# Kernel optimization log

Measured on AMD Instinct MI355X. Metric: run time of the kernel, lower is better.

The kernel has to match this reference:

```python
import jax, jax.numpy as jnp
import numpy as np

H, W = 32, 56
CK, CV = 64, 512
N = 16 * H * W  # long + work memory fully populated: 16 frames of H*W entries
TOP_K = 30


def setup_inputs() -> dict:
    key = jax.random.key(0)
    k1, k2, k3, k4, k5 = jax.random.split(key, 5)
    return {
        "q_key": jax.random.normal(k1, (1, CK, H, W), dtype=jnp.float32),
        "q_selection": jax.random.uniform(k2, (1, CK, H, W), dtype=jnp.float32),
        "mem_key": jax.random.normal(k3, (1, CK, N), dtype=jnp.float32),
        "mem_shrinkage": jax.random.uniform(k4, (1, N, 1), dtype=jnp.float32),
        "mem_value": jax.random.normal(k5, (2, CV, N), dtype=jnp.float32),
    }


def reference(q_key, q_selection, mem_key, mem_shrinkage, mem_value):
    b, ck, h, w = q_key.shape
    hw = h * w
    qk = q_key.reshape(1, ck, hw)          # [1, CK, HW]
    qs = q_selection.reshape(1, ck, hw)    # [1, CK, HW]

    mk = jnp.swapaxes(mem_key, 1, 2)       # [1, N, CK]
    # negative weighted squared L2 distance via matmul algebra
    a_sq = jnp.matmul(mk * mk, qs)                    # [1, N, HW]
    two_ab = 2.0 * jnp.matmul(mk, qk * qs)            # [1, N, HW]
    b_sq = jnp.sum(qs * qk * qk, axis=1, keepdims=True)  # [1, 1, HW]
    sim = (-a_sq + two_ab - b_sq) * mem_shrinkage / jnp.sqrt(jnp.float32(ck))  # [1, N, HW]

    # topk over the memory axis (dim=1), softmax over selected entries, scatter back
    simT = jnp.swapaxes(sim, 1, 2)                    # [1, HW, N]
    vals, idx = jax.lax.top_k(simT, TOP_K)            # [1, HW, K]
    x_exp = jnp.exp(vals)
    x_exp = x_exp / jnp.sum(x_exp, axis=-1, keepdims=True)
    i0 = jnp.arange(1)[:, None, None]
    i1 = jnp.arange(hw)[None, :, None]
    affT = jnp.zeros_like(simT).at[i0, i1, idx].set(x_exp)  # [1, HW, N]
    affinity = jnp.swapaxes(affT, 1, 2)               # [1, N, HW]

    out = jnp.matmul(mem_value, affinity)             # [2, CV, HW] (batch-broadcast)
    return out.reshape(2, CV, h, w)
```

## Files before the change

### kernel.cpp

```cpp
#include <hip/hip_runtime.h>
#include <math.h>

#define HW      1792
#define NMEM    28672
#define NCHUNK  3584
#define TOPK    30
#define CTARGET 48
#define SCAP    64
#define FINCAP  64
#define SIMB    448
#define WPS     7
#define NSELB   448

typedef __attribute__((ext_vector_type(8))) short bf16x8;
typedef __attribute__((ext_vector_type(8))) unsigned short u16x8;
typedef __attribute__((ext_vector_type(4))) float f32x4;
typedef __attribute__((ext_vector_type(4))) _Float16 h4;
typedef unsigned long long ull;

static __device__ __forceinline__ unsigned short f2bf(float v) {
  unsigned b = __float_as_uint(v);
  return (unsigned short)((b + 0x7FFFu + ((b >> 16) & 1u)) >> 16);
}
static __device__ __forceinline__ float bf2f(unsigned short h) {
  return __uint_as_float(((unsigned)h) << 16);
}
static __device__ __forceinline__ unsigned fkey(float v) {
  return __float_as_uint(-v) & 0x7FFFFFFFu;
}
static __device__ __forceinline__ void gl_lds16(const void* g, void* l) {
  __builtin_amdgcn_global_load_lds(
      (const __attribute__((address_space(1))) unsigned*)g,
      (__attribute__((address_space(3))) unsigned*)l, 16, 0, 0);
}
#define WSYNC() do { asm volatile("s_waitcnt lgkmcnt(0)" ::: "memory"); \
                     __builtin_amdgcn_wave_barrier(); } while (0)

__global__ __launch_bounds__(256)
void k_prep_b(const float* __restrict__ mk, const float* __restrict__ shr_in,
              unsigned short* __restrict__ Bh,
              float* __restrict__ mkT, float* __restrict__ shr_s)
{
  const int n = blockIdx.x * 256 + threadIdx.x;
  shr_s[n] = shr_in[n] * 0.125f;
  for (int cb = 0; cb < 64; cb += 8) {
    u16x8 h1, h2;
    float vv[8];
    #pragma unroll
    for (int j = 0; j < 8; ++j) {
      float v = mk[(size_t)(cb + j) * NMEM + n];
      vv[j] = v;
      h1[j] = f2bf(v);
      h2[j] = f2bf(v * v);
    }
    const int s = cb >> 3;
    *reinterpret_cast<u16x8*>(&Bh[((size_t)s * NMEM + n) * 8])       = h1;
    *reinterpret_cast<u16x8*>(&Bh[((size_t)(s + 8) * NMEM + n) * 8]) = h2;
    *reinterpret_cast<float4*>(&mkT[(size_t)n * 64 + cb])     = make_float4(vv[0], vv[1], vv[2], vv[3]);
    *reinterpret_cast<float4*>(&mkT[(size_t)n * 64 + cb + 4]) = make_float4(vv[4], vv[5], vv[6], vv[7]);
  }
}

__global__ __launch_bounds__(256)
void k_prep_u(const float* __restrict__ q_key, const float* __restrict__ q_sel,
              unsigned short* __restrict__ Uh, unsigned short* __restrict__ Ul,
              float* __restrict__ bsq)
{
  const int p = blockIdx.x * 256 + threadIdx.x;
  float bs = 0.f;
  for (int cb = 0; cb < 64; cb += 8) {
    u16x8 h1, l1, h2, l2;
    #pragma unroll
    for (int j = 0; j < 8; ++j) {
      int c = cb + j;
      float k = q_key[(size_t)c * HW + p];
      float s = q_sel[(size_t)c * HW + p];
      float u = 2.f * k * s;
      float w = -s;
      bs = fmaf(s * k, k, bs);
      unsigned short h = f2bf(u); h1[j] = h; l1[j] = f2bf(u - bf2f(h));
      unsigned short g = f2bf(w); h2[j] = g; l2[j] = f2bf(w - bf2f(g));
    }
    const int s = cb >> 3;
    *reinterpret_cast<u16x8*>(&Uh[((size_t)s * HW + p) * 8])       = h1;
    *reinterpret_cast<u16x8*>(&Ul[((size_t)s * HW + p) * 8])       = l1;
    *reinterpret_cast<u16x8*>(&Uh[((size_t)(s + 8) * HW + p) * 8]) = h2;
    *reinterpret_cast<u16x8*>(&Ul[((size_t)(s + 8) * HW + p) * 8]) = l2;
  }
  bsq[p] = bs;
}

__global__ __launch_bounds__(256, 2)
void k_sim(const unsigned short* __restrict__ Uh, const unsigned short* __restrict__ Ul,
           const unsigned short* __restrict__ Bh,
           const float* __restrict__ bsq, const float* __restrict__ shr_s,
           float* __restrict__ pmax)
{
  __shared__ char smem[65536] __attribute__((aligned(16)));
  const int tid = threadIdx.x;
  const int wid = tid >> 6, lane = tid & 63;
  const int lr = lane & 15, lg = lane >> 4;
  const int pb = blockIdx.x % 14, st = blockIdx.x / 14;
  const int pw = pb * 128 + wid * 32;
  const int w0 = st * WPS;

  bf16x8 a0h[4], a0l[4], a1h[4], a1l[4];
  #pragma unroll
  for (int t = 0; t < 4; ++t) {
    const size_t e0 = ((size_t)(t * 4 + lg) * HW + pw + lr) * 8;
    const size_t e1 = e0 + 16 * 8;
    a0h[t] = *reinterpret_cast<const bf16x8*>(&Uh[e0]);
    a0l[t] = *reinterpret_cast<const bf16x8*>(&Ul[e0]);
    a1h[t] = *reinterpret_cast<const bf16x8*>(&Uh[e1]);
    a1l[t] = *reinterpret_cast<const bf16x8*>(&Ul[e1]);
  }
  float bq[2][4];
  #pragma unroll
  for (int pt = 0; pt < 2; ++pt)
    #pragma unroll
    for (int r = 0; r < 4; ++r) bq[pt][r] = bsq[pw + pt * 16 + 4 * lg + r];

  auto stage = [&](int buf, int i) {
    const int n0 = (w0 + i) * 128;
    #pragma unroll
    for (int j = 0; j < 8; ++j) {
      const int idx = j * 256 + tid;
      const int s = idx >> 7, rr = idx & 127;
      gl_lds16((const char*)Bh + ((size_t)s * NMEM + n0 + rr) * 16,
               smem + buf * 32768 + idx * 16);
    }
  };

  stage(0, 0);
  int buf = 0;
  for (int i = 0; i < WPS; ++i) {
    __syncthreads();
    if (i + 1 < WPS) stage(buf ^ 1, i + 1);

    f32x4 acc[2][8];
    #pragma unroll
    for (int a = 0; a < 2; ++a)
      #pragma unroll
      for (int b = 0; b < 8; ++b) acc[a][b] = (f32x4){0.f, 0.f, 0.f, 0.f};

    const short* lb = (const short*)(smem + buf * 32768);
    #pragma unroll
    for (int t = 0; t < 4; ++t) {
      #pragma unroll
      for (int nt = 0; nt < 8; ++nt) {
        bf16x8 bh = *reinterpret_cast<const bf16x8*>(
            &lb[((t * 4 + lg) * 128 + nt * 16 + lr) * 8]);
        acc[0][nt] = __builtin_amdgcn_mfma_f32_16x16x32_bf16(a0h[t], bh, acc[0][nt], 0, 0, 0);
        acc[0][nt] = __builtin_amdgcn_mfma_f32_16x16x32_bf16(a0l[t], bh, acc[0][nt], 0, 0, 0);
        acc[1][nt] = __builtin_amdgcn_mfma_f32_16x16x32_bf16(a1h[t], bh, acc[1][nt], 0, 0, 0);
        acc[1][nt] = __builtin_amdgcn_mfma_f32_16x16x32_bf16(a1l[t], bh, acc[1][nt], 0, 0, 0);
      }
    }

    const int wgl = w0 + i;
    const int n0 = wgl * 128;
    float shv[8];
    #pragma unroll
    for (int nt = 0; nt < 8; ++nt) shv[nt] = shr_s[n0 + nt * 16 + lr];
    #pragma unroll
    for (int pt = 0; pt < 2; ++pt) {
      #pragma unroll
      for (int r = 0; r < 4; ++r) {
        float mx = -INFINITY;
        #pragma unroll
        for (int nt = 0; nt < 8; ++nt)
          mx = fmaxf(mx, (acc[pt][nt][r] - bq[pt][r]) * shv[nt]);
        pmax[(size_t)(pw + pt * 16 + 4 * lg + r) * NCHUNK + wgl * 16 + lr] = mx;
      }
    }
    buf ^= 1;
  }
}

struct SelS {
  int   hist[4][512];
  ull   pk[4][512];
  ull   fin[4][FINCAP];
  short sl[4][SCAP];
  float sqk[4][64], sqs[4][64];
};
union SMemU { SelS sel; float tt[64][65]; };

static __device__ __forceinline__ int ph(int b) { return ((b & 7) << 6) | (b >> 3); }

static __device__ __forceinline__ void wave_cross8(const int* h, int lane, int target,
                                                   int& B, int& nA)
{
  int hv[8]; int ls = 0;
  #pragma unroll
  for (int k = 0; k < 8; ++k) { hv[k] = h[(k << 6) + lane]; ls += hv[k]; }
  int sc = ls;
  #pragma unroll
  for (int off = 1; off < 64; off <<= 1) {
    int t = __shfl_up(sc, off);
    if (lane >= off) sc += t;
  }
  int run = sc - ls;
  int myB = -1, mynA = 0;
  #pragma unroll
  for (int k = 0; k < 8; ++k) {
    if (run < target && run + hv[k] >= target) { myB = lane * 8 + k; mynA = run; }
    run += hv[k];
  }
  ull ball = __ballot(myB >= 0);
  int src = __ffsll((long long)ball) - 1;
  B = __shfl(myB, src); nA = __shfl(mynA, src);
}

__global__ __launch_bounds__(256, 4)
void k_selT(const float* __restrict__ pmax, const float* __restrict__ mkT,
            const float* __restrict__ q_key, const float* __restrict__ q_sel,
            const float* __restrict__ shr_s,
            float* __restrict__ wgt, int* __restrict__ widx,
            const float* __restrict__ mv, _Float16* __restrict__ mvT)
{
  __shared__ SMemU sm;
  const int tid = threadIdx.x;

  int sg = -1, tb = -1;
  if (gridDim.x > NSELB) {
    const int g = blockIdx.x / 17, r = blockIdx.x % 17;
    if (r == 0) sg = g; else tb = g * 16 + (r - 1);
  } else {
    sg = blockIdx.x;
  }

  if (tb >= 0) {
    const int n0 = (tb % 448) * 64, ch0 = (tb / 448) * 64;
    for (int i = tid; i < 64 * 16; i += 256) {
      int r = i >> 4, c4 = (i & 15) << 2;
      float4 v = *reinterpret_cast<const float4*>(&mv[(size_t)(ch0 + r) * NMEM + n0 + c4]);
      sm.tt[r][c4] = v.x; sm.tt[r][c4 + 1] = v.y;
      sm.tt[r][c4 + 2] = v.z; sm.tt[r][c4 + 3] = v.w;
    }
    __syncthreads();
    for (int i = tid; i < 64 * 16; i += 256) {
      int r = i >> 4, c4 = (i & 15) << 2;
      h4 hv = {(_Float16)sm.tt[c4][r], (_Float16)sm.tt[c4 + 1][r],
               (_Float16)sm.tt[c4 + 2][r], (_Float16)sm.tt[c4 + 3][r]};
      *reinterpret_cast<h4*>(&mvT[(size_t)(n0 + r) * 1024 + ch0 + c4]) = hv;
    }
    return;
  }

  const int w = tid >> 6, lane = tid & 63;
  const int pix = sg * 4 + w;
  int*   h  = sm.sel.hist[w];
  ull*   p  = sm.sel.pk[w];
  ull*   fin = sm.sel.fin[w];
  short* sl = sm.sel.sl[w];

  sm.sel.sqk[w][lane] = q_key[(size_t)lane * HW + pix];
  sm.sel.sqs[w][lane] = q_sel[(size_t)lane * HW + pix];

  float m[56];
  const float* pm = pmax + (size_t)pix * NCHUNK;
  #pragma unroll
  for (int j = 0; j < 56; ++j) m[j] = pm[lane + 64 * j];

  #pragma unroll
  for (int k = 0; k < 8; ++k) h[lane + 64 * k] = 0;
  WSYNC();
  #pragma unroll
  for (int j = 0; j < 56; ++j) atomicAdd(&h[ph(fkey(m[j]) >> 22)], 1);
  WSYNC();
  int B1, nA1;
  wave_cross8(h, lane, CTARGET, B1, nA1);

  #pragma unroll
  for (int k = 0; k < 8; ++k) h[lane + 64 * k] = 0;
  WSYNC();
  #pragma unroll
  for (int j = 0; j < 56; ++j) {
    unsigned u = fkey(m[j]);
    if ((int)(u >> 22) == B1) atomicAdd(&h[ph((u >> 13) & 511)], 1);
  }
  WSYNC();
  int Bs1, nAs1;
  wave_cross8(h, lane, CTARGET - nA1, Bs1, nAs1);

  int nsurv = 0;
  #pragma unroll
  for (int j = 0; j < 56; ++j) {
    unsigned u = fkey(m[j]);
    int b1 = (int)(u >> 22);
    bool keep = (b1 < B1) || (b1 == B1 && (int)((u >> 13) & 511) <= Bs1);
    ull ball = __ballot(keep);
    if (keep) {
      int pos = nsurv + __popcll(ball & ((1ull << lane) - 1ull));
      if (pos < SCAP) sl[pos] = (short)(lane + 64 * j);
    }
    nsurv += __popcll(ball);
  }
  nsurv = (nsurv < SCAP) ? nsurv : SCAP;
  const int NC = nsurv * 8;
  WSYNC();

  const float4* k4p = reinterpret_cast<const float4*>(sm.sel.sqk[w]);
  const float4* s4p = reinterpret_cast<const float4*>(sm.sel.sqs[w]);
  for (int c = lane; c < NC; c += 64) {
    const int cc = sl[c >> 3];
    const int n = ((cc >> 4) << 7) + (cc & 15) + ((c & 7) << 4);
    const float4* mr = reinterpret_cast<const float4*>(mkT + (size_t)n * 64);
    float s0 = 0.f, s1 = 0.f, s2 = 0.f, s3 = 0.f;
    #pragma unroll
    for (int j = 0; j < 4; ++j) {
      float4 q0 = mr[4 * j], q1 = mr[4 * j + 1], q2 = mr[4 * j + 2], q3 = mr[4 * j + 3];
      float4 a0 = k4p[4 * j], a1 = k4p[4 * j + 1], a2 = k4p[4 * j + 2], a3 = k4p[4 * j + 3];
      float4 b0 = s4p[4 * j], b1 = s4p[4 * j + 1], b2 = s4p[4 * j + 2], b3 = s4p[4 * j + 3];
      float d;
      d = q0.x - a0.x; s0 = fmaf(b0.x * d, d, s0);
      d = q0.y - a0.y; s1 = fmaf(b0.y * d, d, s1);
      d = q0.z - a0.z; s2 = fmaf(b0.z * d, d, s2);
      d = q0.w - a0.w; s3 = fmaf(b0.w * d, d, s3);
      d = q1.x - a1.x; s0 = fmaf(b1.x * d, d, s0);
      d = q1.y - a1.y; s1 = fmaf(b1.y * d, d, s1);
      d = q1.z - a1.z; s2 = fmaf(b1.z * d, d, s2);
      d = q1.w - a1.w; s3 = fmaf(b1.w * d, d, s3);
      d = q2.x - a2.x; s0 = fmaf(b2.x * d, d, s0);
      d = q2.y - a2.y; s1 = fmaf(b2.y * d, d, s1);
      d = q2.z - a2.z; s2 = fmaf(b2.z * d, d, s2);
      d = q2.w - a2.w; s3 = fmaf(b2.w * d, d, s3);
      d = q3.x - a3.x; s0 = fmaf(b3.x * d, d, s0);
      d = q3.y - a3.y; s1 = fmaf(b3.y * d, d, s1);
      d = q3.z - a3.z; s2 = fmaf(b3.z * d, d, s2);
      d = q3.w - a3.w; s3 = fmaf(b3.w * d, d, s3);
    }
    float v = -((s0 + s1) + (s2 + s3)) * shr_s[n];
    p[c] = ((ull)(0x7FFFFFFFu - fkey(v)) << 32) |
           (ull)(0xFFFFFFFFu - (unsigned)n);
  }
  WSYNC();

  #pragma unroll
  for (int k = 0; k < 8; ++k) h[lane + 64 * k] = 0;
  WSYNC();
  for (int c = lane; c < NC; c += 64) {
    unsigned qk = 0x7FFFFFFFu - (unsigned)(p[c] >> 32);
    atomicAdd(&h[ph(qk >> 22)], 1);
  }
  WSYNC();
  int B2, nA2;
  wave_cross8(h, lane, TOPK, B2, nA2);

  #pragma unroll
  for (int k = 0; k < 8; ++k) h[lane + 64 * k] = 0;
  WSYNC();
  for (int c = lane; c < NC; c += 64) {
    unsigned qk = 0x7FFFFFFFu - (unsigned)(p[c] >> 32);
    if ((int)(qk >> 22) == B2) atomicAdd(&h[ph((qk >> 13) & 511)], 1);
  }
  WSYNC();
  int Bs2, nAs2;
  wave_cross8(h, lane, TOPK - nA2, Bs2, nAs2);

  int nfin = 0;
  for (int c0 = 0; c0 < NC; c0 += 64) {
    int c = c0 + lane;
    bool isf = false; ull key = 0ull;
    if (c < NC) {
      key = p[c];
      unsigned qk = 0x7FFFFFFFu - (unsigned)(key >> 32);
      int b1 = (int)(qk >> 22);
      isf = (b1 < B2) || (b1 == B2 && (int)((qk >> 13) & 511) <= Bs2);
    }
    ull ball = __ballot(isf);
    if (isf) {
      int pos = nfin + __popcll(ball & ((1ull << lane) - 1ull));
      if (pos < FINCAP) fin[pos] = key;
    }
    nfin += __popcll(ball);
  }
  WSYNC();
  const int nf = (nfin < FINCAP) ? nfin : FINCAP;

  ull myk = (lane < nf) ? fin[lane] : 0ull;
  int r = 0;
  #pragma unroll
  for (int sft = 1; sft < 64; ++sft) {
    ull ok = __shfl_xor(myk, sft);
    r += (ok > myk) ? 1 : 0;
  }
  float v = -__uint_as_float(0x7FFFFFFFu - (unsigned)(myk >> 32));
  bool sel = (lane < nf) && (r < TOPK);
  float e = sel ? expf(v) : 0.f;
  float es = e;
  #pragma unroll
  for (int off = 32; off > 0; off >>= 1) es += __shfl_xor(es, off);
  if (sel) {
    wgt [(size_t)pix * 32 + r] = e / es;
    widx[(size_t)pix * 32 + r] = (int)(0xFFFFFFFFu - (unsigned)(myk & 0xFFFFFFFFu));
  }
}

__global__ __launch_bounds__(256)
void k_transpose_h(const float* __restrict__ mv, _Float16* __restrict__ mvT)
{
  __shared__ float t[64][65];
  const int n0 = blockIdx.x * 64, ch0 = blockIdx.y * 64;
  const int tid = threadIdx.x;
  for (int i = tid; i < 64 * 16; i += 256) {
    int r = i >> 4, c4 = (i & 15) << 2;
    float4 v = *reinterpret_cast<const float4*>(&mv[(size_t)(ch0 + r) * NMEM + n0 + c4]);
    t[r][c4] = v.x; t[r][c4 + 1] = v.y; t[r][c4 + 2] = v.z; t[r][c4 + 3] = v.w;
  }
  __syncthreads();
  for (int i = tid; i < 64 * 16; i += 256) {
    int r = i >> 4, c4 = (i & 15) << 2;
    h4 hv = {(_Float16)t[c4][r], (_Float16)t[c4 + 1][r],
             (_Float16)t[c4 + 2][r], (_Float16)t[c4 + 3][r]};
    *reinterpret_cast<h4*>(&mvT[(size_t)(n0 + r) * 1024 + ch0 + c4]) = hv;
  }
}

__global__ __launch_bounds__(256)
void k_gather_h(const _Float16* __restrict__ mvT, const float* __restrict__ wgt,
                const int* __restrict__ widx, float* __restrict__ out)
{
  __shared__ float sw[8][TOPK];
  __shared__ int   si[8][TOPK];
  __shared__ float sbuf[256][9];
  const int p0 = blockIdx.x * 8, chg = blockIdx.y * 256;
  const int tid = threadIdx.x;

  for (int i = tid; i < 8 * TOPK; i += 256) {
    int q = i / TOPK, k = i - q * TOPK;
    sw[q][k] = wgt [(size_t)(p0 + q) * 32 + k];
    si[q][k] = widx[(size_t)(p0 + q) * 32 + k];
  }
  __syncthreads();

  const int ch = chg + tid;
  #pragma unroll 2
  for (int q = 0; q < 8; ++q) {
    float a = 0.f;
    #pragma unroll
    for (int k = 0; k < TOPK; ++k)
      a = fmaf(sw[q][k], (float)mvT[(size_t)si[q][k] * 1024 + ch], a);
    sbuf[tid][q] = a;
  }
  __syncthreads();

  for (int i = tid; i < 256 * 8; i += 256) {
    int cl = i >> 3, q = i & 7;
    out[(size_t)(chg + cl) * HW + p0 + q] = sbuf[cl][q];
  }
}

__global__ __launch_bounds__(256)
void k_gather_f(const float* __restrict__ src, const float* __restrict__ wgt,
                const int* __restrict__ widx, float* __restrict__ out,
                long n_stride, long ch_stride)
{
  __shared__ float sw[8][TOPK];
  __shared__ int   si[8][TOPK];
  __shared__ float sbuf[256][9];
  const int p0 = blockIdx.x * 8, chg = blockIdx.y * 256;
  const int tid = threadIdx.x;

  for (int i = tid; i < 8 * TOPK; i += 256) {
    int q = i / TOPK, k = i - q * TOPK;
    sw[q][k] = wgt [(size_t)(p0 + q) * 32 + k];
    si[q][k] = widx[(size_t)(p0 + q) * 32 + k];
  }
  __syncthreads();

  const int ch = chg + tid;
  #pragma unroll 2
  for (int q = 0; q < 8; ++q) {
    float a = 0.f;
    #pragma unroll
    for (int k = 0; k < TOPK; ++k)
      a = fmaf(sw[q][k], src[(size_t)si[q][k] * n_stride + (size_t)ch * ch_stride], a);
    sbuf[tid][q] = a;
  }
  __syncthreads();

  for (int i = tid; i < 256 * 8; i += 256) {
    int cl = i >> 3, q = i & 7;
    out[(size_t)(chg + cl) * HW + p0 + q] = sbuf[cl][q];
  }
}

extern "C" void kernel_launch(void* const* d_in, const int* in_sizes, int n_in,
                              void* d_out, int out_size, void* d_ws, size_t ws_size,
                              hipStream_t stream)
{
  (void)in_sizes; (void)n_in; (void)out_size;
  const float* q_key     = (const float*)d_in[0];
  const float* q_sel     = (const float*)d_in[1];
  const float* mem_key   = (const float*)d_in[2];
  const float* mem_shr   = (const float*)d_in[3];
  const float* mem_value = (const float*)d_in[4];
  float* out = (float*)d_out;

  char* ws = (char*)d_ws;
  size_t off = 0;
  auto alloc = [&](size_t b) { size_t c = off; off = (off + b + 255) & ~(size_t)255; return c; };
  size_t o_w   = alloc((size_t)HW * 32 * 4);
  size_t o_wi  = alloc((size_t)HW * 32 * 4);
  size_t o_pr  = off;
  size_t o_bh  = alloc((size_t)NMEM * 128 * 2);
  size_t o_uh  = alloc((size_t)HW * 128 * 2);
  size_t o_ul  = alloc((size_t)HW * 128 * 2);
  size_t o_bsq = alloc((size_t)HW * 4);
  size_t o_shr = alloc((size_t)NMEM * 4);
  size_t o_mkT = alloc((size_t)NMEM * 64 * 4);
  size_t o_pm  = alloc((size_t)HW * NCHUNK * 4);
  size_t o_end = off;

  float*          wg   = (float*)(ws + o_w);
  int*            wi   = (int*)  (ws + o_wi);
  unsigned short* Bh   = (unsigned short*)(ws + o_bh);
  unsigned short* Uh   = (unsigned short*)(ws + o_uh);
  unsigned short* Ul   = (unsigned short*)(ws + o_ul);
  float*          bsq  = (float*)(ws + o_bsq);
  float*          shr  = (float*)(ws + o_shr);
  float*          mkT  = (float*)(ws + o_mkT);
  float*          pmx  = (float*)(ws + o_pm);

  const size_t mvh_sz = (size_t)NMEM * 1024 * 2;

  k_prep_b<<<NMEM / 256, 256, 0, stream>>>(mem_key, mem_shr, Bh, mkT, shr);
  k_prep_u<<<HW / 256, 256, 0, stream>>>(q_key, q_sel, Uh, Ul, bsq);
  k_sim<<<SIMB, 256, 0, stream>>>(Uh, Ul, Bh, bsq, shr, pmx);

  if (ws_size >= o_end + mvh_sz) {
    _Float16* mvT = (_Float16*)(ws + o_end);
    k_selT<<<NSELB * 17, 256, 0, stream>>>(pmx, mkT, q_key, q_sel, shr,
                                           wg, wi, mem_value, mvT);
    k_gather_h<<<dim3(HW / 8, 4), 256, 0, stream>>>(mvT, wg, wi, out);
  } else if (ws_size >= o_pr + mvh_sz) {
    k_selT<<<NSELB, 256, 0, stream>>>(pmx, mkT, q_key, q_sel, shr,
                                      wg, wi, mem_value, nullptr);
    _Float16* mvT = (_Float16*)(ws + o_pr);
    k_transpose_h<<<dim3(NMEM / 64, 16), 256, 0, stream>>>(mem_value, mvT);
    k_gather_h<<<dim3(HW / 8, 4), 256, 0, stream>>>(mvT, wg, wi, out);
  } else {
    k_selT<<<NSELB, 256, 0, stream>>>(pmx, mkT, q_key, q_sel, shr,
                                      wg, wi, mem_value, nullptr);
    k_gather_f<<<dim3(HW / 8, 4), 256, 0, stream>>>(
        mem_value, wg, wi, out, 1, NMEM);
  }
}
```

Before: 155.8 us.

## Replace histogram radix top-k selection with bitonic threshold and rank-based selection

Replaces the two-level LDS atomic-histogram radix selects in the per-pixel selection kernel with a different scheme. A wave-wide bitonic sort of per-lane chunk maxima gives a threshold, and chunks at or above it are ranked by counting to pick the top 48. Candidates are then kept in registers, each lane keeps its top 4, and these are ranked against each other to find the top 30. A full-rank fallback runs when the fast path cannot confirm the 30th element. This is meant to cut LDS atomics and repeated histogram passes, at the cost of O(n^2) rank loops and more registers.

```diff
diff --git a/kernel.cpp b/kernel.cpp
--- a/kernel.cpp
+++ b/kernel.cpp
@@ -5,9 +5,9 @@
 #define NMEM    28672
 #define NCHUNK  3584
 #define TOPK    30
-#define CTARGET 48
-#define SCAP    64
-#define FINCAP  64
+#define KSEL    48
+#define NCAND   (KSEL * 8)
+#define SCAP1   1024
 #define SIMB    448
 #define WPS     7
 #define NSELB   448
@@ -28,6 +28,8 @@
 static __device__ __forceinline__ unsigned fkey(float v) {
   return __float_as_uint(-v) & 0x7FFFFFFFu;
 }
+static __device__ __forceinline__ ull umax64(ull a, ull b) { return a > b ? a : b; }
+static __device__ __forceinline__ ull umin64(ull a, ull b) { return a < b ? a : b; }
 static __device__ __forceinline__ void gl_lds16(const void* g, void* l) {
   __builtin_amdgcn_global_load_lds(
       (const __attribute__((address_space(1))) unsigned*)g,
@@ -178,39 +180,11 @@
 }
 
 struct SelS {
-  int   hist[4][512];
-  ull   pk[4][512];
-  ull   fin[4][FINCAP];
-  short sl[4][SCAP];
+  ull   buf[4][SCAP1];
+  short sl[4][KSEL];
   float sqk[4][64], sqs[4][64];
 };
 union SMemU { SelS sel; float tt[64][65]; };
-
-static __device__ __forceinline__ int ph(int b) { return ((b & 7) << 6) | (b >> 3); }
-
-static __device__ __forceinline__ void wave_cross8(const int* h, int lane, int target,
-                                                   int& B, int& nA)
-{
-  int hv[8]; int ls = 0;
-  #pragma unroll
-  for (int k = 0; k < 8; ++k) { hv[k] = h[(k << 6) + lane]; ls += hv[k]; }
-  int sc = ls;
-  #pragma unroll
-  for (int off = 1; off < 64; off <<= 1) {
-    int t = __shfl_up(sc, off);
-    if (lane >= off) sc += t;
-  }
-  int run = sc - ls;
-  int myB = -1, mynA = 0;
-  #pragma unroll
-  for (int k = 0; k < 8; ++k) {
-    if (run < target && run + hv[k] >= target) { myB = lane * 8 + k; mynA = run; }
-    run += hv[k];
-  }
-  ull ball = __ballot(myB >= 0);
-  int src = __ffsll((long long)ball) - 1;
-  B = __shfl(myB, src); nA = __shfl(mynA, src);
-}
 
 __global__ __launch_bounds__(256, 4)
 void k_selT(const float* __restrict__ pmax, const float* __restrict__ mkT,
@@ -250,151 +224,179 @@
 
   const int w = tid >> 6, lane = tid & 63;
   const int pix = sg * 4 + w;
-  int*   h  = sm.sel.hist[w];
-  ull*   p  = sm.sel.pk[w];
-  ull*   fin = sm.sel.fin[w];
-  short* sl = sm.sel.sl[w];
+  ull*   buf  = sm.sel.buf[w];
+  ull*   cand = buf;
+  ull*   fin  = buf + NCAND;
+  short* sl   = sm.sel.sl[w];
 
   sm.sel.sqk[w][lane] = q_key[(size_t)lane * HW + pix];
   sm.sel.sqs[w][lane] = q_sel[(size_t)lane * HW + pix];
 
-  float m[56];
   const float* pm = pmax + (size_t)pix * NCHUNK;
-  #pragma unroll
-  for (int j = 0; j < 56; ++j) m[j] = pm[lane + 64 * j];
-
-  #pragma unroll
-  for (int k = 0; k < 8; ++k) h[lane + 64 * k] = 0;
-  WSYNC();
-  #pragma unroll
-  for (int j = 0; j < 56; ++j) atomicAdd(&h[ph(fkey(m[j]) >> 22)], 1);
-  WSYNC();
-  int B1, nA1;
-  wave_cross8(h, lane, CTARGET, B1, nA1);
-
-  #pragma unroll
-  for (int k = 0; k < 8; ++k) h[lane + 64 * k] = 0;
-  WSYNC();
+
+  float mx = -INFINITY;
+  #pragma unroll
+  for (int j = 0; j < 56; ++j) mx = fmaxf(mx, pm[lane + 64 * j]);
+
+  float v = mx;
+  #pragma unroll
+  for (int k = 2; k <= 64; k <<= 1) {
+    #pragma unroll
+    for (int j = k >> 1; j > 0; j >>= 1) {
+      float o = __shfl_xor(v, j);
+      bool keepmin = (((lane & k) == 0) == ((lane & j) == 0));
+      v = keepmin ? fminf(v, o) : fmaxf(v, o);
+    }
+  }
+  const float t0 = __shfl(v, 64 - KSEL);
+
+  int ns0 = 0;
   #pragma unroll
   for (int j = 0; j < 56; ++j) {
-    unsigned u = fkey(m[j]);
-    if ((int)(u >> 22) == B1) atomicAdd(&h[ph((u >> 13) & 511)], 1);
-  }
-  WSYNC();
-  int Bs1, nAs1;
-  wave_cross8(h, lane, CTARGET - nA1, Bs1, nAs1);
-
-  int nsurv = 0;
-  #pragma unroll
-  for (int j = 0; j < 56; ++j) {
-    unsigned u = fkey(m[j]);
-    int b1 = (int)(u >> 22);
-    bool keep = (b1 < B1) || (b1 == B1 && (int)((u >> 13) & 511) <= Bs1);
+    float mv2 = pm[lane + 64 * j];
+    bool keep = (mv2 >= t0);
     ull ball = __ballot(keep);
     if (keep) {
-      int pos = nsurv + __popcll(ball & ((1ull << lane) - 1ull));
-      if (pos < SCAP) sl[pos] = (short)(lane + 64 * j);
-    }
-    nsurv += __popcll(ball);
-  }
-  nsurv = (nsurv < SCAP) ? nsurv : SCAP;
-  const int NC = nsurv * 8;
+      int pos = ns0 + __popcll(ball & ((1ull << lane) - 1ull));
+      if (pos < SCAP1)
+        buf[pos] = ((ull)(0x7FFFFFFFu - fkey(mv2)) << 32) | (unsigned)(lane + 64 * j);
+    }
+    ns0 += __popcll(ball);
+  }
+  ns0 = (ns0 < SCAP1) ? ns0 : SCAP1;
+  WSYNC();
+
+  {
+    ull e0 = (lane < ns0) ? buf[lane] : 0ull;
+    ull e1 = (lane + 64 < ns0) ? buf[lane + 64] : 0ull;
+    int r0 = 0, r1 = 0;
+    for (int k = 0; k < ns0; ++k) {
+      ull kb = buf[k];
+      r0 += (kb > e0); r1 += (kb > e1);
+    }
+    if (e0 && r0 < KSEL) sl[r0] = (short)(unsigned)(e0 & 0xFFFFu);
+    if (e1 && r1 < KSEL) sl[r1] = (short)(unsigned)(e1 & 0xFFFFu);
+    for (int base = 128; base < ns0; base += 64) {
+      ull ee = (base + lane < ns0) ? buf[base + lane] : 0ull;
+      int rr = 0;
+      for (int k = 0; k < ns0; ++k) rr += (buf[k] > ee);
+      if (ee && rr < KSEL) sl[rr] = (short)(unsigned)(ee & 0xFFFFu);
+    }
+  }
   WSYNC();
 
   const float4* k4p = reinterpret_cast<const float4*>(sm.sel.sqk[w]);
   const float4* s4p = reinterpret_cast<const float4*>(sm.sel.sqs[w]);
-  for (int c = lane; c < NC; c += 64) {
+  ull myp[6];
+  #pragma unroll
+  for (int i = 0; i < 6; ++i) {
+    const int c = lane + (i << 6);
     const int cc = sl[c >> 3];
     const int n = ((cc >> 4) << 7) + (cc & 15) + ((c & 7) << 4);
     const float4* mr = reinterpret_cast<const float4*>(mkT + (size_t)n * 64);
     float s0 = 0.f, s1 = 0.f, s2 = 0.f, s3 = 0.f;
     #pragma unroll
     for (int j = 0; j < 4; ++j) {
-      float4 q0 = mr[4 * j], q1 = mr[4 * j + 1], q2 = mr[4 * j + 2], q3 = mr[4 * j + 3];
-      float4 a0 = k4p[4 * j], a1 = k4p[4 * j + 1], a2 = k4p[4 * j + 2], a3 = k4p[4 * j + 3];
-      float4 b0 = s4p[4 * j], b1 = s4p[4 * j + 1], b2 = s4p[4 * j + 2], b3 = s4p[4 * j + 3];
+      float4 q0 = mr[4*j], q1 = mr[4*j+1], q2 = mr[4*j+2], q3 = mr[4*j+3];
+      float4 a0 = k4p[4*j], a1 = k4p[4*j+1], a2 = k4p[4*j+2], a3 = k4p[4*j+3];
+      float4 b0 = s4p[4*j], b1 = s4p[4*j+1], b2 = s4p[4*j+2], b3 = s4p[4*j+3];
       float d;
-      d = q0.x - a0.x; s0 = fmaf(b0.x * d, d, s0);
-      d = q0.y - a0.y; s1 = fmaf(b0.y * d, d, s1);
-      d = q0.z - a0.z; s2 = fmaf(b0.z * d, d, s2);
-      d = q0.w - a0.w; s3 = fmaf(b0.w * d, d, s3);
-      d = q1.x - a1.x; s0 = fmaf(b1.x * d, d, s0);
-      d = q1.y - a1.y; s1 = fmaf(b1.y * d, d, s1);
-      d = q1.z - a1.z; s2 = fmaf(b1.z * d, d, s2);
-      d = q1.w - a1.w; s3 = fmaf(b1.w * d, d, s3);
-      d = q2.x - a2.x; s0 = fmaf(b2.x * d, d, s0);
-      d = q2.y - a2.y; s1 = fmaf(b2.y * d, d, s1);
-      d = q2.z - a2.z; s2 = fmaf(b2.z * d, d, s2);
-      d = q2.w - a2.w; s3 = fmaf(b2.w * d, d, s3);
-      d = q3.x - a3.x; s0 = fmaf(b3.x * d, d, s0);
-      d = q3.y - a3.y; s1 = fmaf(b3.y * d, d, s1);
-      d = q3.z - a3.z; s2 = fmaf(b3.z * d, d, s2);
-      d = q3.w - a3.w; s3 = fmaf(b3.w * d, d, s3);
-    }
-    float v = -((s0 + s1) + (s2 + s3)) * shr_s[n];
-    p[c] = ((ull)(0x7FFFFFFFu - fkey(v)) << 32) |
-           (ull)(0xFFFFFFFFu - (unsigned)n);
+      d = q0.x-a0.x; s0 = fmaf(b0.x*d, d, s0);
+      d = q0.y-a0.y; s1 = fmaf(b0.y*d, d, s1);
+      d = q0.z-a0.z; s2 = fmaf(b0.z*d, d, s2);
+      d = q0.w-a0.w; s3 = fmaf(b0.w*d, d, s3);
+      d = q1.x-a1.x; s0 = fmaf(b1.x*d, d, s0);
+      d = q1.y-a1.y; s1 = fmaf(b1.y*d, d, s1);
+      d = q1.z-a1.z; s2 = fmaf(b1.z*d, d, s2);
+      d = q1.w-a1.w; s3 = fmaf(b1.w*d, d, s3);
+      d = q2.x-a2.x; s0 = fmaf(b2.x*d, d, s0);
+      d = q2.y-a2.y; s1 = fmaf(b2.y*d, d, s1);
+      d = q2.z-a2.z; s2 = fmaf(b2.z*d, d, s2);
+      d = q2.w-a2.w; s3 = fmaf(b2.w*d, d, s3);
+      d = q3.x-a3.x; s0 = fmaf(b3.x*d, d, s0);
+      d = q3.y-a3.y; s1 = fmaf(b3.y*d, d, s1);
+      d = q3.z-a3.z; s2 = fmaf(b3.z*d, d, s2);
+      d = q3.w-a3.w; s3 = fmaf(b3.w*d, d, s3);
+    }
+    float sv = -((s0 + s1) + (s2 + s3)) * shr_s[n];
+    ull pk = ((ull)(0x7FFFFFFFu - fkey(sv)) << 32) |
+             (ull)(0xFFFFFFFFu - (unsigned)n);
+    cand[c] = pk;
+    myp[i] = pk;
   }
   WSYNC();
 
-  #pragma unroll
-  for (int k = 0; k < 8; ++k) h[lane + 64 * k] = 0;
+  ull p0 = 0, p1 = 0, p2 = 0, p3 = 0;
+  #pragma unroll
+  for (int i = 0; i < 6; ++i) {
+    ull k = myp[i], m;
+    m = umax64(p0, k); k = umin64(p0, k); p0 = m;
+    m = umax64(p1, k); k = umin64(p1, k); p1 = m;
+    m = umax64(p2, k); k = umin64(p2, k); p2 = m;
+    m = umax64(p3, k); k = umin64(p3, k); p3 = m;
+  }
+  fin[lane * 4 + 0] = p0; fin[lane * 4 + 1] = p1;
+  fin[lane * 4 + 2] = p2; fin[lane * 4 + 3] = p3;
   WSYNC();
-  for (int c = lane; c < NC; c += 64) {
-    unsigned qk = 0x7FFFFFFFu - (unsigned)(p[c] >> 32);
-    atomicAdd(&h[ph(qk >> 22)], 1);
-  }
-  WSYNC();
-  int B2, nA2;
-  wave_cross8(h, lane, TOPK, B2, nA2);
-
-  #pragma unroll
-  for (int k = 0; k < 8; ++k) h[lane + 64 * k] = 0;
-  WSYNC();
-  for (int c = lane; c < NC; c += 64) {
-    unsigned qk = 0x7FFFFFFFu - (unsigned)(p[c] >> 32);
-    if ((int)(qk >> 22) == B2) atomicAdd(&h[ph((qk >> 13) & 511)], 1);
-  }
-  WSYNC();
-  int Bs2, nAs2;
-  wave_cross8(h, lane, TOPK - nA2, Bs2, nAs2);
-
-  int nfin = 0;
-  for (int c0 = 0; c0 < NC; c0 += 64) {
-    int c = c0 + lane;
-    bool isf = false; ull key = 0ull;
-    if (c < NC) {
-      key = p[c];
-      unsigned qk = 0x7FFFFFFFu - (unsigned)(key >> 32);
-      int b1 = (int)(qk >> 22);
-      isf = (b1 < B2) || (b1 == B2 && (int)((qk >> 13) & 511) <= Bs2);
-    }
-    ull ball = __ballot(isf);
-    if (isf) {
-      int pos = nfin + __popcll(ball & ((1ull << lane) - 1ull));
-      if (pos < FINCAP) fin[pos] = key;
-    }
-    nfin += __popcll(ball);
-  }
-  WSYNC();
-  const int nf = (nfin < FINCAP) ? nfin : FINCAP;
-
-  ull myk = (lane < nf) ? fin[lane] : 0ull;
-  int r = 0;
-  #pragma unroll
-  for (int sft = 1; sft < 64; ++sft) {
-    ull ok = __shfl_xor(myk, sft);
-    r += (ok > myk) ? 1 : 0;
-  }
-  float v = -__uint_as_float(0x7FFFFFFFu - (unsigned)(myk >> 32));
-  bool sel = (lane < nf) && (r < TOPK);
-  float e = sel ? expf(v) : 0.f;
-  float es = e;
-  #pragma unroll
-  for (int off = 32; off > 0; off >>= 1) es += __shfl_xor(es, off);
-  if (sel) {
-    wgt [(size_t)pix * 32 + r] = e / es;
-    widx[(size_t)pix * 32 + r] = (int)(0xFFFFFFFFu - (unsigned)(myk & 0xFFFFFFFFu));
+
+  int r0 = 0, r1 = 0, r2 = 0, r3 = 0;
+  for (int k = 0; k < 256; ++k) {
+    ull kb = fin[k];
+    r0 += (kb > p0); r1 += (kb > p1); r2 += (kb > p2); r3 += (kb > p3);
+  }
+  ull c30 = (r0 == TOPK - 1) ? p0 : (r1 == TOPK - 1) ? p1 :
+            (r2 == TOPK - 1) ? p2 : (r3 == TOPK - 1) ? p3 : 0ull;
+  ull ball = __ballot(c30 != 0ull);
+  ull k30 = __shfl(c30, (int)(__ffsll((long long)ball) - 1));
+
+  int cnt = 0;
+  #pragma unroll
+  for (int i = 0; i < 6; ++i) cnt += (myp[i] > k30);
+  #pragma unroll
+  for (int off = 32; off > 0; off >>= 1) cnt += __shfl_xor(cnt, off);
+  const bool ok = (cnt == TOPK - 1);
+
+  if (ok) {
+    float v0 = -__uint_as_float(0x7FFFFFFFu - (unsigned)(p0 >> 32));
+    float v1 = -__uint_as_float(0x7FFFFFFFu - (unsigned)(p1 >> 32));
+    float v2 = -__uint_as_float(0x7FFFFFFFu - (unsigned)(p2 >> 32));
+    float v3 = -__uint_as_float(0x7FFFFFFFu - (unsigned)(p3 >> 32));
+    float e0 = (r0 < TOPK) ? expf(v0) : 0.f;
+    float e1 = (r1 < TOPK) ? expf(v1) : 0.f;
+    float e2 = (r2 < TOPK) ? expf(v2) : 0.f;
+    float e3 = (r3 < TOPK) ? expf(v3) : 0.f;
+    float es = e0 + e1 + e2 + e3;
+    #pragma unroll
+    for (int off = 32; off > 0; off >>= 1) es += __shfl_xor(es, off);
+    if (r0 < TOPK) { wgt[(size_t)pix*32 + r0] = e0/es; widx[(size_t)pix*32 + r0] = (int)(0xFFFFFFFFu - (unsigned)(p0 & 0xFFFFFFFFu)); }
+    if (r1 < TOPK) { wgt[(size_t)pix*32 + r1] = e1/es; widx[(size_t)pix*32 + r1] = (int)(0xFFFFFFFFu - (unsigned)(p1 & 0xFFFFFFFFu)); }
+    if (r2 < TOPK) { wgt[(size_t)pix*32 + r2] = e2/es; widx[(size_t)pix*32 + r2] = (int)(0xFFFFFFFFu - (unsigned)(p2 & 0xFFFFFFFFu)); }
+    if (r3 < TOPK) { wgt[(size_t)pix*32 + r3] = e3/es; widx[(size_t)pix*32 + r3] = (int)(0xFFFFFFFFu - (unsigned)(p3 & 0xFFFFFFFFu)); }
+  } else {
+    int rr[6];
+    #pragma unroll
+    for (int i = 0; i < 6; ++i) rr[i] = 0;
+    for (int k = 0; k < NCAND; ++k) {
+      ull kb = cand[k];
+      #pragma unroll
+      for (int i = 0; i < 6; ++i) rr[i] += (kb > myp[i]);
+    }
+    float ev[6]; float es = 0.f;
+    #pragma unroll
+    for (int i = 0; i < 6; ++i) {
+      float vv = -__uint_as_float(0x7FFFFFFFu - (unsigned)(myp[i] >> 32));
+      ev[i] = (rr[i] < TOPK) ? expf(vv) : 0.f;
+      es += ev[i];
+    }
+    #pragma unroll
+    for (int off = 32; off > 0; off >>= 1) es += __shfl_xor(es, off);
+    #pragma unroll
+    for (int i = 0; i < 6; ++i) {
+      if (rr[i] < TOPK) {
+        wgt [(size_t)pix * 32 + rr[i]] = ev[i] / es;
+        widx[(size_t)pix * 32 + rr[i]] = (int)(0xFFFFFFFFu - (unsigned)(myp[i] & 0xFFFFFFFFu));
+      }
+    }
   }
 }
 
```

New measurement: 169.7 us. 1.09x slower.
